# Kernel optimization log

Measured on AMD Instinct MI355X. Metric: run time of the kernel, lower is better.

Reference implementation:

```python
import jax, jax.numpy as jnp
import numpy as np

B, N, F_IN = 2, 2048, 256
HEADS, F_OUT = 8, 32
NEG_SLOPE = 0.01  # torch F.leaky_relu default


def setup_inputs() -> dict:
    key = jax.random.key(0)
    k1, k2, k3, k4 = jax.random.split(key, 4)
    stdv = 1.0 / np.sqrt(F_OUT * HEADS)
    h = jax.random.normal(k1, (B, N, F_IN), dtype=jnp.float32)
    adj = jax.random.uniform(k2, (B, N, N), dtype=jnp.float32)
    W = jax.random.normal(k3, (F_IN, F_OUT * HEADS), dtype=jnp.float32) * stdv
    a = jax.random.normal(k4, (2 * F_OUT, 1), dtype=jnp.float32) * stdv
    return {"h": h, "adj": adj, "W": W, "a": a}


def reference(h, adj, W, a):
    # adj is accepted by the original forward but never used (dense attention).
    b, n, _ = h.shape
    f = a.shape[0] // 2
    heads = W.shape[1] // f
    Wh = (h @ W).reshape(b, n, heads, f)            # [b,n,h,f]
    a1 = a[:f, 0]                                    # attends to source i
    a2 = a[f:, 0]                                    # attends to target j
    e1 = jnp.einsum('bnhf,f->bhn', Wh, a1)           # [b,h,n]
    e2 = jnp.einsum('bnhf,f->bhn', Wh, a2)           # [b,h,n]
    # e[b,h,i,j] = leaky_relu(a1.Wh_i + a2.Wh_j) == a^T [Wh_i || Wh_j]
    e = jax.nn.leaky_relu(e1[:, :, :, None] + e2[:, :, None, :], NEG_SLOPE)
    att = jax.nn.softmax(e, axis=-1)                 # softmax over neighbors j
    h_prime = jnp.einsum('bhij,bjhf->bihf', att, Wh)  # [b,n,h,f]
    return h_prime.reshape(b, n, heads * f)
```

## Files before the change

### kernel.cpp

```cpp
#include <hip/hip_runtime.h>
#include <math.h>

#define BATCH 2
#define NTOK  2048
#define FIN   256
#define HEADS 8
#define FOUT  32
#define BH    (BATCH*HEADS)
#define NCOL  (HEADS*FOUT)
#define ROWS  (BATCH*NTOK)

typedef _Float16 f16;
typedef _Float16 f16x8 __attribute__((ext_vector_type(8)));
typedef float    f32x4 __attribute__((ext_vector_type(4)));

static const size_t OFF_E1   = 1048576;
static const size_t OFF_E2   = OFF_E1 + 32768;
static const size_t OFF_SKEY = OFF_E2 + 32768;
static const size_t OFF_SIDX = OFF_SKEY + 32768;
static const size_t OFF_W1S  = OFF_SIDX + 32768;
static const size_t OFF_W2S  = OFF_W1S + 32768;
static const size_t OFF_S1   = OFF_W2S + 32768;
static const size_t OFF_P2   = OFF_S1 + 32784;
static const size_t OFF_V1   = OFF_P2 + 32784;
static const size_t OFF_P2V  = OFF_V1 + 16u*2049u*32u;
static const size_t OFF_HHI  = OFF_P2V + 16u*2049u*32u;
static const size_t OFF_HLO  = OFF_HHI + 524288;
static const size_t OFF_WTHI = OFF_HLO + 524288;
static const size_t OFF_WTLO = OFF_WTHI + 32768;
static const size_t OFF_PART = OFF_V1;

__global__ __launch_bounds__(256) void k_split(const float* __restrict__ h,
                                               const float* __restrict__ W,
                                               f16* __restrict__ hhi, f16* __restrict__ hlo,
                                               f16* __restrict__ wthi, f16* __restrict__ wtlo) {
    const int tid = threadIdx.x;
    if (blockIdx.x < 512) {
        const size_t base = ((size_t)blockIdx.x * 256 + tid) * 8;
        const float4 v0 = *(const float4*)(h + base);
        const float4 v1 = *(const float4*)(h + base + 4);
        const float xs[8] = {v0.x,v0.y,v0.z,v0.w,v1.x,v1.y,v1.z,v1.w};
        f16x8 hi8, lo8;
        #pragma unroll
        for (int i = 0; i < 8; ++i) {
            float xv = xs[i] * 16.0f;
            f16 hv = (f16)xv;
            hi8[i] = hv;
            lo8[i] = (f16)(xv - (float)hv);
        }
        *(f16x8*)(hhi + base) = hi8;
        *(f16x8*)(hlo + base) = lo8;
    } else {
        const int k0 = (blockIdx.x - 512) * 16;
        const int c  = tid;
        f16x8 hiA, loA, hiB, loB;
        #pragma unroll
        for (int j = 0; j < 8; ++j) {
            float xv = W[(size_t)(k0 + j) * 256 + c] * 4096.0f;
            f16 hv = (f16)xv;
            hiA[j] = hv; loA[j] = (f16)(xv - (float)hv);
        }
        #pragma unroll
        for (int j = 0; j < 8; ++j) {
            float xv = W[(size_t)(k0 + 8 + j) * 256 + c] * 4096.0f;
            f16 hv = (f16)xv;
            hiB[j] = hv; loB[j] = (f16)(xv - (float)hv);
        }
        f16* pd = wthi + (size_t)c * 256 + k0;
        f16* pe = wtlo + (size_t)c * 256 + k0;
        *(f16x8*)pd = hiA; *(f16x8*)(pd + 8) = hiB;
        *(f16x8*)pe = loA; *(f16x8*)(pe + 8) = loB;
    }
}

__global__ __launch_bounds__(256) void k_mm(const f16* __restrict__ hhi, const f16* __restrict__ hlo,
                                            const f16* __restrict__ wthi, const f16* __restrict__ wtlo,
                                            const float* __restrict__ a,
                                            float* __restrict__ Wh,
                                            float* __restrict__ e1, float* __restrict__ e2) {
    const int tid  = threadIdx.x;
    const int wv   = tid >> 6;
    const int lane = tid & 63;
    const int r    = lane & 15;
    const int q    = lane >> 4;
    const int row0 = blockIdx.x * 16;
    const int col0 = wv * 64;
    const int koff = q * 8;

    const f16* pa_hi = hhi  + (size_t)(row0 + r) * 256 + koff;
    const f16* pa_lo = hlo  + (size_t)(row0 + r) * 256 + koff;
    const f16* pb_hi = wthi + (size_t)(col0 + r) * 256 + koff;
    const f16* pb_lo = wtlo + (size_t)(col0 + r) * 256 + koff;

    f32x4 acc[4];
    #pragma unroll
    for (int t = 0; t < 4; ++t) acc[t] = (f32x4){0.f,0.f,0.f,0.f};

    struct FR { f16x8 ah, al, bh[4], bl[4]; };
    auto ldfr = [&](int ch) {
        FR f;
        const int o = ch * 32;
        f.ah = *(const f16x8*)(pa_hi + o);
        f.al = *(const f16x8*)(pa_lo + o);
        #pragma unroll
        for (int t = 0; t < 4; ++t) {
            f.bh[t] = *(const f16x8*)(pb_hi + t * (16 * 256) + o);
            f.bl[t] = *(const f16x8*)(pb_lo + t * (16 * 256) + o);
        }
        return f;
    };
    auto dom = [&](const FR& f) {
        #pragma unroll
        for (int t = 0; t < 4; ++t) {
            acc[t] = __builtin_amdgcn_mfma_f32_16x16x32_f16(f.ah, f.bh[t], acc[t], 0, 0, 0);
            acc[t] = __builtin_amdgcn_mfma_f32_16x16x32_f16(f.ah, f.bl[t], acc[t], 0, 0, 0);
            acc[t] = __builtin_amdgcn_mfma_f32_16x16x32_f16(f.al, f.bh[t], acc[t], 0, 0, 0);
        }
    };

    FR fa = ldfr(0);
    FR fb = ldfr(1);
    #pragma unroll
    for (int ch = 0; ch < 8; ch += 2) {
        dom(fa);
        if (ch + 2 < 8) fa = ldfr(ch + 2);
        dom(fb);
        if (ch + 3 < 8) fb = ldfr(ch + 3);
    }

    const float SC = 1.0f / 65536.0f;
    #pragma unroll
    for (int t = 0; t < 4; ++t) acc[t] *= SC;

    #pragma unroll
    for (int t = 0; t < 4; ++t)
        #pragma unroll
        for (int g = 0; g < 4; ++g)
            Wh[(size_t)(row0 + q * 4 + g) * 256 + col0 + t * 16 + r] = acc[t][g];

    const float av10 = a[r], av11 = a[16 + r], av20 = a[32 + r], av21 = a[48 + r];
    float p1[8], p2[8];
    #pragma unroll
    for (int hp = 0; hp < 2; ++hp)
        #pragma unroll
        for (int g = 0; g < 4; ++g) {
            p1[hp * 4 + g] = acc[2 * hp][g] * av10 + acc[2 * hp + 1][g] * av11;
            p2[hp * 4 + g] = acc[2 * hp][g] * av20 + acc[2 * hp + 1][g] * av21;
        }
    #pragma unroll
    for (int m = 1; m < 16; m <<= 1) {
        #pragma unroll
        for (int i = 0; i < 8; ++i) {
            p1[i] += __shfl_xor(p1[i], m, 64);
            p2[i] += __shfl_xor(p2[i], m, 64);
        }
    }
    if (r == 0) {
        #pragma unroll
        for (int hp = 0; hp < 2; ++hp)
            #pragma unroll
            for (int g = 0; g < 4; ++g) {
                const int row  = row0 + q * 4 + g;
                const int b    = row >> 11;
                const int n    = row & (NTOK - 1);
                const int head = wv * 2 + hp;
                e1[(b * HEADS + head) * NTOK + n] = p1[hp * 4 + g];
                e2[(b * HEADS + head) * NTOK + n] = p2[hp * 4 + g];
            }
    }
}

__device__ __forceinline__ unsigned long long sortkey(float f, int j) {
    unsigned int b = __float_as_uint(f);
    unsigned int u = (b & 0x80000000u) ? ~b : (b | 0x80000000u);
    return ((unsigned long long)u << 32) | (unsigned int)(NTOK - 1 - j);
}

__global__ __launch_bounds__(256) void k_rank8(const float* __restrict__ e2g,
                                               int* __restrict__ partial) {
    __shared__ alignas(16) unsigned long long ch[256];
    const int tid = threadIdx.x;
    const int bh  = blockIdx.x;
    const int jt  = blockIdx.y;
    const int kt  = blockIdx.z;
    const int kbase = kt * 256;
    ch[tid] = sortkey(e2g[bh * NTOK + kbase + tid], kbase + tid);
    __syncthreads();

    const int j = jt * 256 + tid;
    const unsigned long long my = sortkey(e2g[bh * NTOK + j], j);
    int rank = 0;
    const ulonglong2* c2 = (const ulonglong2*)ch;
    #pragma unroll 8
    for (int q = 0; q < 128; ++q) {
        ulonglong2 v = c2[q];
        rank += (v.x > my);
        rank += (v.y > my);
    }
    partial[(kt * BH + bh) * NTOK + j] = rank;
}

__global__ __launch_bounds__(256) void k_scatter(const float* __restrict__ e2g,
                                                 const int* __restrict__ partial,
                                                 float* __restrict__ skey,
                                                 int* __restrict__ sidx,
                                                 float* __restrict__ w1s,
                                                 float* __restrict__ w2s) {
    const int tid = threadIdx.x;
    const int bh  = blockIdx.x;
    const int jt  = blockIdx.y;
    const int j   = jt * 256 + tid;
    int rank = 0;
    #pragma unroll
    for (int kt = 0; kt < 8; ++kt)
        rank += partial[(kt * BH + bh) * NTOK + j];
    const float my = e2g[bh * NTOK + j];
    skey[bh * NTOK + rank] = my;
    sidx[bh * NTOK + rank] = j;
    w1s[bh * NTOK + rank]  = expf(my);
    w2s[bh * NTOK + rank]  = expf(0.01f * my);
}

__global__ __launch_bounds__(1024) void k_vscan(const float* __restrict__ Wh,
                                                const int* __restrict__ sidx,
                                                const float* __restrict__ w1s,
                                                const float* __restrict__ w2s,
                                                float* __restrict__ V1,
                                                float* __restrict__ P2V,
                                                float* __restrict__ S1,
                                                float* __restrict__ P2) {
    __shared__ float4 wtot[16];
    __shared__ float4 woff[16];
    const int t    = threadIdx.x;
    const int lane = t & 63;
    const int wv   = t >> 6;
    const int fg   = blockIdx.x;
    const int bh   = blockIdx.y;
    const int z    = blockIdx.z;
    const int b    = bh >> 3;
    const int hh   = bh & 7;
    const float* wsrc = z ? w2s : w1s;

    const int j0 = 2 * t;
    float4 v0, v1;
    if (fg < 8) {
        int sj0 = sidx[bh * NTOK + j0];
        int sj1 = sidx[bh * NTOK + j0 + 1];
        float w0 = wsrc[bh * NTOK + j0];
        float w1 = wsrc[bh * NTOK + j0 + 1];
        float4 g0 = *(const float4*)(Wh + (size_t)(b * NTOK + sj0) * NCOL + hh * FOUT + fg * 4);
        float4 g1 = *(const float4*)(Wh + (size_t)(b * NTOK + sj1) * NCOL + hh * FOUT + fg * 4);
        v0 = make_float4(w0 * g0.x, w0 * g0.y, w0 * g0.z, w0 * g0.w);
        v1 = make_float4(w1 * g1.x, w1 * g1.y, w1 * g1.z, w1 * g1.w);
    } else {
        v0 = make_float4(wsrc[bh * NTOK + j0],     0.f, 0.f, 0.f);
        v1 = make_float4(wsrc[bh * NTOK + j0 + 1], 0.f, 0.f, 0.f);
    }

    float4 s = make_float4(v0.x + v1.x, v0.y + v1.y, v0.z + v1.z, v0.w + v1.w);
    #pragma unroll
    for (int d = 1; d < 64; d <<= 1) {
        float ux = __shfl_up(s.x, (unsigned)d, 64);
        float uy = __shfl_up(s.y, (unsigned)d, 64);
        float uz = __shfl_up(s.z, (unsigned)d, 64);
        float uw = __shfl_up(s.w, (unsigned)d, 64);
        if (lane >= d) { s.x += ux; s.y += uy; s.z += uz; s.w += uw; }
    }
    float4 pair = make_float4(v0.x + v1.x, v0.y + v1.y, v0.z + v1.z, v0.w + v1.w);
    float4 excl = make_float4(s.x - pair.x, s.y - pair.y, s.z - pair.z, s.w - pair.w);
    if (lane == 63) wtot[wv] = s;
    __syncthreads();
    if (t < 16) {
        float4 ws = wtot[t];
        float4 inc = ws;
        #pragma unroll
        for (int d = 1; d < 16; d <<= 1) {
            float ux = __shfl_up(inc.x, (unsigned)d, 16);
            float uy = __shfl_up(inc.y, (unsigned)d, 16);
            float uz = __shfl_up(inc.z, (unsigned)d, 16);
            float uw = __shfl_up(inc.w, (unsigned)d, 16);
            if ((t & 15) >= d) { inc.x += ux; inc.y += uy; inc.z += uz; inc.w += uw; }
        }
        woff[t] = make_float4(inc.x - ws.x, inc.y - ws.y, inc.z - ws.z, inc.w - ws.w);
    }
    __syncthreads();

    float4 base = woff[wv];
    float4 i0 = make_float4(base.x + excl.x + v0.x, base.y + excl.y + v0.y,
                            base.z + excl.z + v0.z, base.w + excl.w + v0.w);
    float4 i1 = make_float4(i0.x + v1.x, i0.y + v1.y, i0.z + v1.z, i0.w + v1.w);

    if (fg < 8) {
        float* dst = z ? P2V : V1;
        float* plane = dst + ((size_t)bh * 8 + fg) * (2049u * 4u);
        *(float4*)(plane + (size_t)(j0 + 1) * 4) = i0;
        *(float4*)(plane + (size_t)(j0 + 2) * 4) = i1;
        if (t == 0)
            *(float4*)plane = make_float4(0.f,0.f,0.f,0.f);
    } else {
        float* dst = z ? P2 : S1;
        dst[bh * 2049 + j0 + 1] = i0.x;
        dst[bh * 2049 + j0 + 2] = i1.x;
        if (t == 0) dst[bh * 2049] = 0.f;
    }
}

__global__ __launch_bounds__(256) void k_out(const float* __restrict__ skey,
                                             const float* __restrict__ e1g,
                                             const float* __restrict__ S1,
                                             const float* __restrict__ P2,
                                             const float* __restrict__ V1,
                                             const float* __restrict__ P2V,
                                             float* __restrict__ out) {
    __shared__ float keys[NTOK];
    const int tid = threadIdx.x;
    const int it  = blockIdx.x;
    const int bh  = blockIdx.y;
    const int b   = bh >> 3;
    const int hh  = bh & 7;
    #pragma unroll
    for (int q = 0; q < 8; ++q)
        keys[q * 256 + tid] = skey[bh * NTOK + q * 256 + tid];
    __syncthreads();

    const int i  = it * 32 + (tid >> 3);
    const int fg = tid & 7;
    const float e1v = e1g[bh * NTOK + i];
    const float th  = -e1v;
    int lo = 0, hi = NTOK;
    while (lo < hi) {
        int mid = (lo + hi) >> 1;
        if (keys[mid] > th) lo = mid + 1; else hi = mid;
    }
    const int k = lo;
    const float A = expf(e1v);
    const float C = expf(0.01f * e1v);
    const float s1  = S1[bh * 2049 + k];
    const float p2k = P2[bh * 2049 + k];
    const float p2t = P2[bh * 2049 + 2048];
    const float l   = A * s1 + C * (p2t - p2k);
    const float inv = 1.0f / l;
    const float* v1p  = V1  + ((size_t)bh * 8 + fg) * (2049u * 4u);
    const float* p2vp = P2V + ((size_t)bh * 8 + fg) * (2049u * 4u);
    float4 v1   = *(const float4*)(v1p  + (size_t)k * 4);
    float4 p2v  = *(const float4*)(p2vp + (size_t)k * 4);
    float4 p2vt = *(const float4*)(p2vp + (size_t)2048 * 4);
    float4 o;
    o.x = (A * v1.x + C * (p2vt.x - p2v.x)) * inv;
    o.y = (A * v1.y + C * (p2vt.y - p2v.y)) * inv;
    o.z = (A * v1.z + C * (p2vt.z - p2v.z)) * inv;
    o.w = (A * v1.w + C * (p2vt.w - p2v.w)) * inv;
    *(float4*)(out + (size_t)(b * NTOK + i) * NCOL + hh * FOUT + fg * 4) = o;
}

extern "C" void kernel_launch(void* const* d_in, const int* in_sizes, int n_in,
                              void* d_out, int out_size, void* d_ws, size_t ws_size,
                              hipStream_t stream) {
    const float* h = (const float*)d_in[0];
    const float* W = (const float*)d_in[2];
    const float* a = (const float*)d_in[3];
    float* out = (float*)d_out;
    float* ws  = (float*)d_ws;

    float* Wh   = ws;
    float* e1   = ws + OFF_E1;
    float* e2   = ws + OFF_E2;
    float* skey = ws + OFF_SKEY;
    int*   sidx = (int*)(ws + OFF_SIDX);
    float* w1s  = ws + OFF_W1S;
    float* w2s  = ws + OFF_W2S;
    float* S1   = ws + OFF_S1;
    float* P2   = ws + OFF_P2;
    float* V1   = ws + OFF_V1;
    float* P2V  = ws + OFF_P2V;
    f16*   hhi  = (f16*)(ws + OFF_HHI);
    f16*   hlo  = (f16*)(ws + OFF_HLO);
    f16*   wthi = (f16*)(ws + OFF_WTHI);
    f16*   wtlo = (f16*)(ws + OFF_WTLO);
    int*   part = (int*)(ws + OFF_PART);

    k_split  <<<528,              256, 0, stream>>>(h, W, hhi, hlo, wthi, wtlo);
    k_mm     <<<256,              256, 0, stream>>>(hhi, hlo, wthi, wtlo, a, Wh, e1, e2);
    k_rank8  <<<dim3(BH, 8, 8),   256, 0, stream>>>(e2, part);
    k_scatter<<<dim3(BH, 8),      256, 0, stream>>>(e2, part, skey, sidx, w1s, w2s);
    k_vscan  <<<dim3(9, BH, 2),  1024, 0, stream>>>(Wh, sidx, w1s, w2s, V1, P2V, S1, P2);
    k_out    <<<dim3(NTOK/32, BH),256, 0, stream>>>(skey, e1, S1, P2, V1, P2V, out);
}
```

Baseline: 124.1 us.

## Fuse fp16 split into matmul, register-block rank counting, merge vscan passes

Removes the separate k_split kernel: k_mm now reads fp32 h and W directly and does the hi/lo fp16 split in registers before the MFMAs, using 512 threads with one wave per head. k_rank8 has each thread rank four keys against the shared chunk, so the grid shrinks and the LDS reads are reused four times. k_vscan does both the w1 and w2 scans in one block with a loop, so the Wh gather is loaded once instead of twice. Together these cut launches and intermediate traffic. In exchange, W is re-converted redundantly by every block with strided scalar loads, and vscan has fewer blocks and longer serial work.

```diff
diff --git a/kernel.cpp b/kernel.cpp
--- a/kernel.cpp
+++ b/kernel.cpp
@@ -24,149 +24,92 @@
 static const size_t OFF_P2   = OFF_S1 + 32784;
 static const size_t OFF_V1   = OFF_P2 + 32784;
 static const size_t OFF_P2V  = OFF_V1 + 16u*2049u*32u;
-static const size_t OFF_HHI  = OFF_P2V + 16u*2049u*32u;
-static const size_t OFF_HLO  = OFF_HHI + 524288;
-static const size_t OFF_WTHI = OFF_HLO + 524288;
-static const size_t OFF_WTLO = OFF_WTHI + 32768;
 static const size_t OFF_PART = OFF_V1;
 
-__global__ __launch_bounds__(256) void k_split(const float* __restrict__ h,
-                                               const float* __restrict__ W,
-                                               f16* __restrict__ hhi, f16* __restrict__ hlo,
-                                               f16* __restrict__ wthi, f16* __restrict__ wtlo) {
-    const int tid = threadIdx.x;
-    if (blockIdx.x < 512) {
-        const size_t base = ((size_t)blockIdx.x * 256 + tid) * 8;
-        const float4 v0 = *(const float4*)(h + base);
-        const float4 v1 = *(const float4*)(h + base + 4);
-        const float xs[8] = {v0.x,v0.y,v0.z,v0.w,v1.x,v1.y,v1.z,v1.w};
-        f16x8 hi8, lo8;
-        #pragma unroll
-        for (int i = 0; i < 8; ++i) {
-            float xv = xs[i] * 16.0f;
-            f16 hv = (f16)xv;
-            hi8[i] = hv;
-            lo8[i] = (f16)(xv - (float)hv);
-        }
-        *(f16x8*)(hhi + base) = hi8;
-        *(f16x8*)(hlo + base) = lo8;
-    } else {
-        const int k0 = (blockIdx.x - 512) * 16;
-        const int c  = tid;
-        f16x8 hiA, loA, hiB, loB;
-        #pragma unroll
-        for (int j = 0; j < 8; ++j) {
-            float xv = W[(size_t)(k0 + j) * 256 + c] * 4096.0f;
-            f16 hv = (f16)xv;
-            hiA[j] = hv; loA[j] = (f16)(xv - (float)hv);
-        }
-        #pragma unroll
-        for (int j = 0; j < 8; ++j) {
-            float xv = W[(size_t)(k0 + 8 + j) * 256 + c] * 4096.0f;
-            f16 hv = (f16)xv;
-            hiB[j] = hv; loB[j] = (f16)(xv - (float)hv);
-        }
-        f16* pd = wthi + (size_t)c * 256 + k0;
-        f16* pe = wtlo + (size_t)c * 256 + k0;
-        *(f16x8*)pd = hiA; *(f16x8*)(pd + 8) = hiB;
-        *(f16x8*)pe = loA; *(f16x8*)(pe + 8) = loB;
-    }
-}
-
-__global__ __launch_bounds__(256) void k_mm(const f16* __restrict__ hhi, const f16* __restrict__ hlo,
-                                            const f16* __restrict__ wthi, const f16* __restrict__ wtlo,
-                                            const float* __restrict__ a,
+__global__ __launch_bounds__(512) void k_mm(const float* __restrict__ h,
+                                            const float* __restrict__ W,
+                                            const float* __restrict__ av,
                                             float* __restrict__ Wh,
                                             float* __restrict__ e1, float* __restrict__ e2) {
     const int tid  = threadIdx.x;
-    const int wv   = tid >> 6;
+    const int hh   = tid >> 6;
     const int lane = tid & 63;
     const int r    = lane & 15;
     const int q    = lane >> 4;
     const int row0 = blockIdx.x * 16;
-    const int col0 = wv * 64;
-    const int koff = q * 8;
-
-    const f16* pa_hi = hhi  + (size_t)(row0 + r) * 256 + koff;
-    const f16* pa_lo = hlo  + (size_t)(row0 + r) * 256 + koff;
-    const f16* pb_hi = wthi + (size_t)(col0 + r) * 256 + koff;
-    const f16* pb_lo = wtlo + (size_t)(col0 + r) * 256 + koff;
-
-    f32x4 acc[4];
-    #pragma unroll
-    for (int t = 0; t < 4; ++t) acc[t] = (f32x4){0.f,0.f,0.f,0.f};
-
-    struct FR { f16x8 ah, al, bh[4], bl[4]; };
-    auto ldfr = [&](int ch) {
-        FR f;
-        const int o = ch * 32;
-        f.ah = *(const f16x8*)(pa_hi + o);
-        f.al = *(const f16x8*)(pa_lo + o);
-        #pragma unroll
-        for (int t = 0; t < 4; ++t) {
-            f.bh[t] = *(const f16x8*)(pb_hi + t * (16 * 256) + o);
-            f.bl[t] = *(const f16x8*)(pb_lo + t * (16 * 256) + o);
-        }
-        return f;
-    };
-    auto dom = [&](const FR& f) {
-        #pragma unroll
-        for (int t = 0; t < 4; ++t) {
-            acc[t] = __builtin_amdgcn_mfma_f32_16x16x32_f16(f.ah, f.bh[t], acc[t], 0, 0, 0);
-            acc[t] = __builtin_amdgcn_mfma_f32_16x16x32_f16(f.ah, f.bl[t], acc[t], 0, 0, 0);
-            acc[t] = __builtin_amdgcn_mfma_f32_16x16x32_f16(f.al, f.bh[t], acc[t], 0, 0, 0);
-        }
-    };
-
-    FR fa = ldfr(0);
-    FR fb = ldfr(1);
-    #pragma unroll
-    for (int ch = 0; ch < 8; ch += 2) {
-        dom(fa);
-        if (ch + 2 < 8) fa = ldfr(ch + 2);
-        dom(fb);
-        if (ch + 3 < 8) fb = ldfr(ch + 3);
+    const int colA = hh * 32;
+
+    const float* pa = h + (size_t)(row0 + r) * FIN + q * 8;
+    const float HS = 16.0f, WS = 4096.0f;
+
+    f32x4 acc[2];
+    acc[0] = (f32x4){0.f,0.f,0.f,0.f};
+    acc[1] = (f32x4){0.f,0.f,0.f,0.f};
+
+    for (int ks = 0; ks < 8; ++ks) {
+        const int kb = ks * 32;
+        const float4 a0 = *(const float4*)(pa + kb);
+        const float4 a1 = *(const float4*)(pa + kb + 4);
+        const float ax[8] = {a0.x,a0.y,a0.z,a0.w,a1.x,a1.y,a1.z,a1.w};
+        f16x8 ahi, alo;
+        #pragma unroll
+        for (int j = 0; j < 8; ++j) {
+            float xv = ax[j] * HS;
+            f16 hv = (f16)xv;
+            ahi[j] = hv; alo[j] = (f16)(xv - (float)hv);
+        }
+        f16x8 bhi[2], blo[2];
+        #pragma unroll
+        for (int t = 0; t < 2; ++t) {
+            const float* pb = W + (size_t)(kb + q * 8) * NCOL + colA + t * 16 + r;
+            #pragma unroll
+            for (int j = 0; j < 8; ++j) {
+                float xv = pb[(size_t)j * NCOL] * WS;
+                f16 hv = (f16)xv;
+                bhi[t][j] = hv; blo[t][j] = (f16)(xv - (float)hv);
+            }
+        }
+        #pragma unroll
+        for (int t = 0; t < 2; ++t) {
+            acc[t] = __builtin_amdgcn_mfma_f32_16x16x32_f16(ahi, bhi[t], acc[t], 0, 0, 0);
+            acc[t] = __builtin_amdgcn_mfma_f32_16x16x32_f16(ahi, blo[t], acc[t], 0, 0, 0);
+            acc[t] = __builtin_amdgcn_mfma_f32_16x16x32_f16(alo, bhi[t], acc[t], 0, 0, 0);
+        }
     }
 
     const float SC = 1.0f / 65536.0f;
-    #pragma unroll
-    for (int t = 0; t < 4; ++t) acc[t] *= SC;
-
-    #pragma unroll
-    for (int t = 0; t < 4; ++t)
+    acc[0] *= SC; acc[1] *= SC;
+
+    #pragma unroll
+    for (int t = 0; t < 2; ++t)
         #pragma unroll
         for (int g = 0; g < 4; ++g)
-            Wh[(size_t)(row0 + q * 4 + g) * 256 + col0 + t * 16 + r] = acc[t][g];
-
-    const float av10 = a[r], av11 = a[16 + r], av20 = a[32 + r], av21 = a[48 + r];
-    float p1[8], p2[8];
-    #pragma unroll
-    for (int hp = 0; hp < 2; ++hp)
+            Wh[(size_t)(row0 + q * 4 + g) * NCOL + colA + t * 16 + r] = acc[t][g];
+
+    const float a10 = av[r], a11 = av[16 + r];
+    const float a20 = av[32 + r], a21 = av[48 + r];
+    float p1[4], p2[4];
+    #pragma unroll
+    for (int g = 0; g < 4; ++g) {
+        p1[g] = acc[0][g] * a10 + acc[1][g] * a11;
+        p2[g] = acc[0][g] * a20 + acc[1][g] * a21;
+    }
+    #pragma unroll
+    for (int m = 1; m < 16; m <<= 1)
         #pragma unroll
         for (int g = 0; g < 4; ++g) {
-            p1[hp * 4 + g] = acc[2 * hp][g] * av10 + acc[2 * hp + 1][g] * av11;
-            p2[hp * 4 + g] = acc[2 * hp][g] * av20 + acc[2 * hp + 1][g] * av21;
-        }
-    #pragma unroll
-    for (int m = 1; m < 16; m <<= 1) {
-        #pragma unroll
-        for (int i = 0; i < 8; ++i) {
-            p1[i] += __shfl_xor(p1[i], m, 64);
-            p2[i] += __shfl_xor(p2[i], m, 64);
-        }
-    }
+            p1[g] += __shfl_xor(p1[g], m, 64);
+            p2[g] += __shfl_xor(p2[g], m, 64);
+        }
     if (r == 0) {
         #pragma unroll
-        for (int hp = 0; hp < 2; ++hp)
-            #pragma unroll
-            for (int g = 0; g < 4; ++g) {
-                const int row  = row0 + q * 4 + g;
-                const int b    = row >> 11;
-                const int n    = row & (NTOK - 1);
-                const int head = wv * 2 + hp;
-                e1[(b * HEADS + head) * NTOK + n] = p1[hp * 4 + g];
-                e2[(b * HEADS + head) * NTOK + n] = p2[hp * 4 + g];
-            }
+        for (int g = 0; g < 4; ++g) {
+            const int row = row0 + q * 4 + g;
+            const int b   = row >> 11;
+            const int n   = row & (NTOK - 1);
+            e1[(b * HEADS + hh) * NTOK + n] = p1[g];
+            e2[(b * HEADS + hh) * NTOK + n] = p2[g];
+        }
     }
 }
 
@@ -181,23 +124,29 @@
     __shared__ alignas(16) unsigned long long ch[256];
     const int tid = threadIdx.x;
     const int bh  = blockIdx.x;
-    const int jt  = blockIdx.y;
-    const int kt  = blockIdx.z;
+    const int kt  = blockIdx.y;
+    const int jh  = blockIdx.z;
     const int kbase = kt * 256;
     ch[tid] = sortkey(e2g[bh * NTOK + kbase + tid], kbase + tid);
     __syncthreads();
 
-    const int j = jt * 256 + tid;
-    const unsigned long long my = sortkey(e2g[bh * NTOK + j], j);
-    int rank = 0;
+    const int j0 = jh * 1024 + tid * 4;
+    const float4 mv = *(const float4*)(e2g + bh * NTOK + j0);
+    const unsigned long long my0 = sortkey(mv.x, j0);
+    const unsigned long long my1 = sortkey(mv.y, j0 + 1);
+    const unsigned long long my2 = sortkey(mv.z, j0 + 2);
+    const unsigned long long my3 = sortkey(mv.w, j0 + 3);
+    int r0 = 0, r1 = 0, r2 = 0, r3 = 0;
     const ulonglong2* c2 = (const ulonglong2*)ch;
     #pragma unroll 8
-    for (int q = 0; q < 128; ++q) {
-        ulonglong2 v = c2[q];
-        rank += (v.x > my);
-        rank += (v.y > my);
-    }
-    partial[(kt * BH + bh) * NTOK + j] = rank;
+    for (int qq = 0; qq < 128; ++qq) {
+        ulonglong2 v = c2[qq];
+        r0 += (v.x > my0) + (v.y > my0);
+        r1 += (v.x > my1) + (v.y > my1);
+        r2 += (v.x > my2) + (v.y > my2);
+        r3 += (v.x > my3) + (v.y > my3);
+    }
+    *(int4*)(partial + (size_t)(kt * BH + bh) * NTOK + j0) = make_int4(r0, r1, r2, r3);
 }
 
 __global__ __launch_bounds__(256) void k_scatter(const float* __restrict__ e2g,
@@ -213,7 +162,7 @@
     int rank = 0;
     #pragma unroll
     for (int kt = 0; kt < 8; ++kt)
-        rank += partial[(kt * BH + bh) * NTOK + j];
+        rank += partial[(size_t)(kt * BH + bh) * NTOK + j];
     const float my = e2g[bh * NTOK + j];
     skey[bh * NTOK + rank] = my;
     sidx[bh * NTOK + rank] = j;
@@ -236,72 +185,77 @@
     const int wv   = t >> 6;
     const int fg   = blockIdx.x;
     const int bh   = blockIdx.y;
-    const int z    = blockIdx.z;
     const int b    = bh >> 3;
     const int hh   = bh & 7;
-    const float* wsrc = z ? w2s : w1s;
-
-    const int j0 = 2 * t;
-    float4 v0, v1;
+    const int j0   = 2 * t;
+
+    const float w1_0 = w1s[bh * NTOK + j0], w1_1 = w1s[bh * NTOK + j0 + 1];
+    const float w2_0 = w2s[bh * NTOK + j0], w2_1 = w2s[bh * NTOK + j0 + 1];
+    float4 g0, g1;
     if (fg < 8) {
-        int sj0 = sidx[bh * NTOK + j0];
-        int sj1 = sidx[bh * NTOK + j0 + 1];
-        float w0 = wsrc[bh * NTOK + j0];
-        float w1 = wsrc[bh * NTOK + j0 + 1];
-        float4 g0 = *(const float4*)(Wh + (size_t)(b * NTOK + sj0) * NCOL + hh * FOUT + fg * 4);
-        float4 g1 = *(const float4*)(Wh + (size_t)(b * NTOK + sj1) * NCOL + hh * FOUT + fg * 4);
-        v0 = make_float4(w0 * g0.x, w0 * g0.y, w0 * g0.z, w0 * g0.w);
-        v1 = make_float4(w1 * g1.x, w1 * g1.y, w1 * g1.z, w1 * g1.w);
+        const int sj0 = sidx[bh * NTOK + j0];
+        const int sj1 = sidx[bh * NTOK + j0 + 1];
+        g0 = *(const float4*)(Wh + (size_t)(b * NTOK + sj0) * NCOL + hh * FOUT + fg * 4);
+        g1 = *(const float4*)(Wh + (size_t)(b * NTOK + sj1) * NCOL + hh * FOUT + fg * 4);
     } else {
-        v0 = make_float4(wsrc[bh * NTOK + j0],     0.f, 0.f, 0.f);
-        v1 = make_float4(wsrc[bh * NTOK + j0 + 1], 0.f, 0.f, 0.f);
-    }
-
-    float4 s = make_float4(v0.x + v1.x, v0.y + v1.y, v0.z + v1.z, v0.w + v1.w);
-    #pragma unroll
-    for (int d = 1; d < 64; d <<= 1) {
-        float ux = __shfl_up(s.x, (unsigned)d, 64);
-        float uy = __shfl_up(s.y, (unsigned)d, 64);
-        float uz = __shfl_up(s.z, (unsigned)d, 64);
-        float uw = __shfl_up(s.w, (unsigned)d, 64);
-        if (lane >= d) { s.x += ux; s.y += uy; s.z += uz; s.w += uw; }
-    }
-    float4 pair = make_float4(v0.x + v1.x, v0.y + v1.y, v0.z + v1.z, v0.w + v1.w);
-    float4 excl = make_float4(s.x - pair.x, s.y - pair.y, s.z - pair.z, s.w - pair.w);
-    if (lane == 63) wtot[wv] = s;
-    __syncthreads();
-    if (t < 16) {
-        float4 ws = wtot[t];
-        float4 inc = ws;
-        #pragma unroll
-        for (int d = 1; d < 16; d <<= 1) {
-            float ux = __shfl_up(inc.x, (unsigned)d, 16);
-            float uy = __shfl_up(inc.y, (unsigned)d, 16);
-            float uz = __shfl_up(inc.z, (unsigned)d, 16);
-            float uw = __shfl_up(inc.w, (unsigned)d, 16);
-            if ((t & 15) >= d) { inc.x += ux; inc.y += uy; inc.z += uz; inc.w += uw; }
-        }
-        woff[t] = make_float4(inc.x - ws.x, inc.y - ws.y, inc.z - ws.z, inc.w - ws.w);
-    }
-    __syncthreads();
-
-    float4 base = woff[wv];
-    float4 i0 = make_float4(base.x + excl.x + v0.x, base.y + excl.y + v0.y,
-                            base.z + excl.z + v0.z, base.w + excl.w + v0.w);
-    float4 i1 = make_float4(i0.x + v1.x, i0.y + v1.y, i0.z + v1.z, i0.w + v1.w);
-
-    if (fg < 8) {
-        float* dst = z ? P2V : V1;
-        float* plane = dst + ((size_t)bh * 8 + fg) * (2049u * 4u);
-        *(float4*)(plane + (size_t)(j0 + 1) * 4) = i0;
-        *(float4*)(plane + (size_t)(j0 + 2) * 4) = i1;
-        if (t == 0)
-            *(float4*)plane = make_float4(0.f,0.f,0.f,0.f);
-    } else {
-        float* dst = z ? P2 : S1;
-        dst[bh * 2049 + j0 + 1] = i0.x;
-        dst[bh * 2049 + j0 + 2] = i1.x;
-        if (t == 0) dst[bh * 2049] = 0.f;
+        g0 = make_float4(1.f, 0.f, 0.f, 0.f);
+        g1 = make_float4(1.f, 0.f, 0.f, 0.f);
+    }
+
+    #pragma unroll 1
+    for (int z = 0; z < 2; ++z) {
+        const float w0  = z ? w2_0 : w1_0;
+        const float w1v = z ? w2_1 : w1_1;
+        float4 v0 = make_float4(w0 * g0.x,  w0 * g0.y,  w0 * g0.z,  w0 * g0.w);
+        float4 v1 = make_float4(w1v * g1.x, w1v * g1.y, w1v * g1.z, w1v * g1.w);
+
+        float4 s = make_float4(v0.x + v1.x, v0.y + v1.y, v0.z + v1.z, v0.w + v1.w);
+        #pragma unroll
+        for (int d = 1; d < 64; d <<= 1) {
+            float ux = __shfl_up(s.x, (unsigned)d, 64);
+            float uy = __shfl_up(s.y, (unsigned)d, 64);
+            float uz = __shfl_up(s.z, (unsigned)d, 64);
+            float uw = __shfl_up(s.w, (unsigned)d, 64);
+            if (lane >= d) { s.x += ux; s.y += uy; s.z += uz; s.w += uw; }
+        }
+        float4 pair = make_float4(v0.x + v1.x, v0.y + v1.y, v0.z + v1.z, v0.w + v1.w);
+        float4 excl = make_float4(s.x - pair.x, s.y - pair.y, s.z - pair.z, s.w - pair.w);
+        if (lane == 63) wtot[wv] = s;
+        __syncthreads();
+        if (t < 16) {
+            float4 ws = wtot[t];
+            float4 inc = ws;
+            #pragma unroll
+            for (int d = 1; d < 16; d <<= 1) {
+                float ux = __shfl_up(inc.x, (unsigned)d, 16);
+                float uy = __shfl_up(inc.y, (unsigned)d, 16);
+                float uz = __shfl_up(inc.z, (unsigned)d, 16);
+                float uw = __shfl_up(inc.w, (unsigned)d, 16);
+                if ((t & 15) >= d) { inc.x += ux; inc.y += uy; inc.z += uz; inc.w += uw; }
+            }
+            woff[t] = make_float4(inc.x - ws.x, inc.y - ws.y, inc.z - ws.z, inc.w - ws.w);
+        }
+        __syncthreads();
+
+        float4 base = woff[wv];
+        float4 i0 = make_float4(base.x + excl.x + v0.x, base.y + excl.y + v0.y,
+                                base.z + excl.z + v0.z, base.w + excl.w + v0.w);
+        float4 i1 = make_float4(i0.x + v1.x, i0.y + v1.y, i0.z + v1.z, i0.w + v1.w);
+
+        if (fg < 8) {
+            float* dst = z ? P2V : V1;
+            float* plane = dst + ((size_t)bh * 8 + fg) * (2049u * 4u);
+            *(float4*)(plane + (size_t)(j0 + 1) * 4) = i0;
+            *(float4*)(plane + (size_t)(j0 + 2) * 4) = i1;
+            if (t == 0)
+                *(float4*)plane = make_float4(0.f, 0.f, 0.f, 0.f);
+        } else {
+            float* dst = z ? P2 : S1;
+            dst[bh * 2049 + j0 + 1] = i0.x;
+            dst[bh * 2049 + j0 + 2] = i1.x;
+            if (t == 0) dst[bh * 2049] = 0.f;
+        }
+        __syncthreads();
     }
 }
 
@@ -373,16 +327,11 @@
     float* P2   = ws + OFF_P2;
     float* V1   = ws + OFF_V1;
     float* P2V  = ws + OFF_P2V;
-    f16*   hhi  = (f16*)(ws + OFF_HHI);
-    f16*   hlo  = (f16*)(ws + OFF_HLO);
-    f16*   wthi = (f16*)(ws + OFF_WTHI);
-    f16*   wtlo = (f16*)(ws + OFF_WTLO);
     int*   part = (int*)(ws + OFF_PART);
 
-    k_split  <<<528,              256, 0, stream>>>(h, W, hhi, hlo, wthi, wtlo);
-    k_mm     <<<256,              256, 0, stream>>>(hhi, hlo, wthi, wtlo, a, Wh, e1, e2);
-    k_rank8  <<<dim3(BH, 8, 8),   256, 0, stream>>>(e2, part);
-    k_scatter<<<dim3(BH, 8),      256, 0, stream>>>(e2, part, skey, sidx, w1s, w2s);
-    k_vscan  <<<dim3(9, BH, 2),  1024, 0, stream>>>(Wh, sidx, w1s, w2s, V1, P2V, S1, P2);
-    k_out    <<<dim3(NTOK/32, BH),256, 0, stream>>>(skey, e1, S1, P2, V1, P2V, out);
-}
+    k_mm     <<<256,               512, 0, stream>>>(h, W, a, Wh, e1, e2);
+    k_rank8  <<<dim3(BH, 8, 2),    256, 0, stream>>>(e2, part);
+    k_scatter<<<dim3(BH, 8),       256, 0, stream>>>(e2, part, skey, sidx, w1s, w2s);
+    k_vscan  <<<dim3(9, BH),      1024, 0, stream>>>(Wh, sidx, w1s, w2s, V1, P2V, S1, P2);
+    k_out    <<<dim3(NTOK/32, BH), 256, 0, stream>>>(skey, e1, S1, P2, V1, P2V, out);
+}
```

Measured after the change: 116.6 us, median of 2. 6.1% less time.
